# Performance work log

Measured on AMD Instinct MI355X. Metric: run time of the kernel, lower is better.

The kernel has to match this reference:

```python
import jax, jax.numpy as jnp
import numpy as np

D_MAIN = 256
D_INT = 512
N_FEAT = 128
N_CLASSES = 10
B = 1024
N_CAND = 100000
CTX = 96
EPS = 1e-5


def layer_norm(x, scale, bias):
    m = jnp.mean(x, axis=-1, keepdims=True)
    v = jnp.var(x, axis=-1, keepdims=True)
    return (x - m) / jnp.sqrt(v + EPS) * scale + bias


def setup_inputs() -> dict:
    key = jax.random.key(0)
    ks = jax.random.split(key, 16)

    def lin_w(k, fi, fo):
        return jax.random.uniform(k, (fi, fo), minval=-1.0, maxval=1.0, dtype=jnp.float32) / np.sqrt(fi)

    def lin_b(k, fi, fo):
        return jax.random.uniform(k, (fo,), minval=-1.0, maxval=1.0, dtype=jnp.float32) / np.sqrt(fi)

    return {
        "x_num": jax.random.normal(ks[0], (B, N_FEAT), dtype=jnp.float32),
        "cand_num": jax.random.normal(ks[1], (N_CAND, N_FEAT), dtype=jnp.float32),
        "cand_y": jax.random.randint(ks[2], (N_CAND,), 0, N_CLASSES),
        "context_size": CTX,
        # input linear (forward_E with encoder_n_blocks=0)
        "W_lin": lin_w(ks[3], N_FEAT, D_MAIN), "b_lin": lin_b(ks[3], N_FEAT, D_MAIN),
        # K projection
        "W_K": lin_w(ks[4], D_MAIN, D_MAIN), "b_K": lin_b(ks[4], D_MAIN, D_MAIN),
        # label embedding Y (init uniform(-1, 1) per reset_parameters)
        "Y_emb": jax.random.uniform(ks[5], (N_CLASSES, D_MAIN), minval=-1.0, maxval=1.0, dtype=jnp.float32),
        # T: Linear(d, d_int) -> ReLU -> Linear(d_int, d, bias=False)
        "T_W1": lin_w(ks[6], D_MAIN, D_INT), "T_b1": lin_b(ks[6], D_MAIN, D_INT),
        "T_W2": lin_w(ks[7], D_INT, D_MAIN),
        # predictor block (LayerNorm -> Linear -> ReLU -> Dropout -> Linear), residual
        "bp_ln_s": jnp.ones((D_MAIN,), jnp.float32), "bp_ln_b": jnp.zeros((D_MAIN,), jnp.float32),
        "bp_W1": lin_w(ks[8], D_MAIN, D_INT), "bp_b1": lin_b(ks[8], D_MAIN, D_INT),
        "bp_W2": lin_w(ks[9], D_INT, D_MAIN), "bp_b2": lin_b(ks[9], D_INT, D_MAIN),
        # head P: LayerNorm -> ReLU -> Linear(d, n_classes)
        "P_ln_s": jnp.ones((D_MAIN,), jnp.float32), "P_ln_b": jnp.zeros((D_MAIN,), jnp.float32),
        "P_W": lin_w(ks[10], D_MAIN, N_CLASSES), "P_b": lin_b(ks[10], D_MAIN, N_CLASSES),
    }


def reference(x_num, cand_num, cand_y, context_size,
              W_lin, b_lin, W_K, b_K, Y_emb, T_W1, T_b1, T_W2,
              bp_ln_s, bp_ln_b, bp_W1, bp_b1, bp_W2, bp_b2,
              P_ln_s, P_ln_b, P_W, P_b):
    # forward_E (encoder_n_blocks=0 => single Linear, normlization is None)
    x = x_num @ W_lin + b_lin                       # [B, d]
    k = x @ W_K + b_K                               # [B, d]

    # candidate keys computed under torch.no_grad in the original -> stop_gradient
    ki_all = jax.lax.stop_gradient((cand_num @ W_lin + b_lin) @ W_K + b_K)  # [N, d]

    # FAISS GpuIndexFlatL2 search: exact L2 top-k (smallest squared distance)
    d2 = (jnp.sum(k * k, axis=-1, keepdims=True)
          - 2.0 * (k @ ki_all.T)
          + jnp.sum(ki_all * ki_all, axis=-1))      # [B, N]
    _, I = jax.lax.top_k(-jax.lax.stop_gradient(d2), context_size)  # [B, C]

    ki = ki_all[I]                                  # [B, C, d]
    diff = k[:, None, :] - ki                       # [B, C, d]
    # NOTE: source computes S = -(-|k|^2 + 2 k.ki - |ki|^2) = +squared distance
    S = jnp.sum(diff * diff, axis=-1)               # [B, C]
    w = jax.nn.softmax(S, axis=-1)                  # context_dropout inactive at inference

    enc_y = Y_emb[cand_y[I]]                        # [B, C, d]
    V = enc_y + jax.nn.relu(diff @ T_W1 + T_b1) @ T_W2
    V = jnp.einsum('bc,bcd->bd', w, V)              # weighted aggregation

    x = x + V
    # predictor block (predictor_n_blocks=1)
    h = layer_norm(x, bp_ln_s, bp_ln_b)
    h = jax.nn.relu(h @ bp_W1 + bp_b1) @ bp_W2 + bp_b2
    x = x + h
    # head P
    return jax.nn.relu(layer_norm(x, P_ln_s, P_ln_b)) @ P_W + P_b
```

## Files before the change

kernel.cpp:

```cpp
#include <hip/hip_runtime.h>
#include <hip/hip_bf16.h>

#define B_ROWS   1024
#define N_FEAT   128
#define D_MAIN   256
#define D_INT    512
#define N_CAND   100000
#define CTX      96
#define N_CLS    10
#define PCHN     8192
#define N2       91808
#define RKEEP    128
#define SCAP     6144
#define SVSTRIDE 16

typedef __attribute__((ext_vector_type(8))) short bf16x8;
typedef __attribute__((ext_vector_type(4))) float f32x4;
typedef unsigned long long u64;

__device__ __forceinline__ float wsum(float v) {
    #pragma unroll
    for (int o = 32; o > 0; o >>= 1) v += __shfl_down(v, o);
    return v;
}
__device__ __forceinline__ float wmax(float v) {
    #pragma unroll
    for (int o = 32; o > 0; o >>= 1) v = fmaxf(v, __shfl_down(v, o));
    return v;
}
__device__ __forceinline__ float blockSum256(float v, float* red) {
    int t = threadIdx.x;
    float s = wsum(v);
    if ((t & 63) == 0) red[t >> 6] = s;
    __syncthreads();
    s = red[0] + red[1] + red[2] + red[3];
    __syncthreads();
    return s;
}
__device__ __forceinline__ float b2f(unsigned short u) {
    return __uint_as_float(((unsigned)u) << 16);
}
__device__ __forceinline__ unsigned short f2b(float f) {
    unsigned x = __float_as_uint(f);
    return (unsigned short)((x + 0x7fff + ((x >> 16) & 1)) >> 16);
}
__device__ __forceinline__ unsigned fkey(float f) {
    unsigned u = __float_as_uint(f);
    return u ^ ((((int)u >> 31)) | 0x80000000u);
}
__device__ __forceinline__ float finv(unsigned k) {
    unsigned u = (k & 0x80000000u) ? (k ^ 0x80000000u) : ~k;
    return __uint_as_float(u);
}
#define SPLIT1(x, hv, lv) { unsigned short _h = f2b(x); hv = (short)_h; lv = (short)f2b((x) - b2f(_h)); }

__global__ __launch_bounds__(256) void encode_batch(
    const float* __restrict__ xn, const float* __restrict__ Wl, const float* __restrict__ bl,
    const float* __restrict__ Wk, const float* __restrict__ bk,
    float* __restrict__ xout, float* __restrict__ kout, float* __restrict__ knorm)
{
    int b = blockIdx.x, t = threadIdx.x;
    __shared__ float si[128], sx[256], red[4];
    if (t < 128) si[t] = xn[b * N_FEAT + t];
    __syncthreads();
    float a = bl[t];
    for (int i = 0; i < 128; ++i) a += si[i] * Wl[i * D_MAIN + t];
    xout[b * D_MAIN + t] = a;
    sx[t] = a;
    __syncthreads();
    float a2 = bk[t];
    for (int i = 0; i < 256; ++i) a2 += sx[i] * Wk[i * D_MAIN + t];
    kout[b * D_MAIN + t] = a2;
    float s = blockSum256(a2 * a2, red);
    if (t == 0) knorm[b] = s;
}

__global__ __launch_bounds__(256) void fuse_weights(
    const float* __restrict__ Wl, const float* __restrict__ Wk,
    const float* __restrict__ bl, const float* __restrict__ bk,
    float* __restrict__ Wf, float* __restrict__ bf)
{
    int i = blockIdx.x, t = threadIdx.x;
    __shared__ float row[256];
    if (i < 128) {
        if (t < 128) row[t] = 0.f;
        row[t % 256] = 0.f;
        __syncthreads();
        if (t < 256) {  }
        row[t] = Wl[i * D_MAIN + t];
        __syncthreads();
        float a = 0.f;
        for (int k = 0; k < 256; ++k) a += row[k] * Wk[k * D_MAIN + t];
        Wf[i * D_MAIN + t] = a;
    } else {
        row[t] = bl[t];
        __syncthreads();
        float a = bk[t];
        for (int k = 0; k < 256; ++k) a += row[k] * Wk[k * D_MAIN + t];
        bf[t] = a;
    }
}

template<bool WRITE_BF16>
__global__ __launch_bounds__(256) void gemm_split3(
    const float* __restrict__ A,
    const unsigned short* __restrict__ Bh,
    const unsigned short* __restrict__ Bl,
    const float* __restrict__ bias,
    float* __restrict__ Cf,
    unsigned short* __restrict__ Cbf,
    int M, int N, int K)
{
    __shared__ __align__(16) short Ash[4096], Asl[4096];
    __shared__ __align__(16) short Bsh[2048], Bsl[2048];
    const int t = threadIdx.x;
    const int bm = blockIdx.x * 128, bn = blockIdx.y * 64;
    const int wave = t >> 6, lane = t & 63;
    const int wm = (wave >> 1) * 64, wn = (wave & 1) * 32;
    const int lr = lane & 15, lkg = lane >> 4;
    f32x4 acc[4][2] = {};
    const int row0 = t >> 2, kg0 = t & 3;
    const int row1 = row0 + 64;
    const int p0 = ((kg0 + (row0 >> 2)) & 3) ^ (row0 & 3);
    const int p1 = ((kg0 + (row1 >> 2)) & 3) ^ (row1 & 3);
    const int gm0 = bm + row0, gm1 = bm + row1;
    const int nB = bn + row0;

    float4 u00, u01, u10, u11;
    bf16x8 bh0, bl0;
    auto prefetch = [&](int kq) {
        float4 z4 = make_float4(0.f, 0.f, 0.f, 0.f); bf16x8 z = {};
        u00 = z4; u01 = z4; u10 = z4; u11 = z4;
        bh0 = z; bl0 = z;
        if (gm0 < M) {
            const float* ap = A + (size_t)gm0 * K + kq + kg0 * 8;
            u00 = *(const float4*)ap; u01 = *(const float4*)(ap + 4);
        }
        if (gm1 < M) {
            const float* ap = A + (size_t)gm1 * K + kq + kg0 * 8;
            u10 = *(const float4*)ap; u11 = *(const float4*)(ap + 4);
        }
        if (nB < N) {
            bh0 = *(const bf16x8*)(Bh + (size_t)nB * K + kq + kg0 * 8);
            bl0 = *(const bf16x8*)(Bl + (size_t)nB * K + kq + kg0 * 8);
        }
    };
    prefetch(0);

    for (int k0 = 0; k0 < K; k0 += 32) {
        bf16x8 a0h, a0l, a1h, a1l;
        SPLIT1(u00.x, a0h[0], a0l[0]); SPLIT1(u00.y, a0h[1], a0l[1]);
        SPLIT1(u00.z, a0h[2], a0l[2]); SPLIT1(u00.w, a0h[3], a0l[3]);
        SPLIT1(u01.x, a0h[4], a0l[4]); SPLIT1(u01.y, a0h[5], a0l[5]);
        SPLIT1(u01.z, a0h[6], a0l[6]); SPLIT1(u01.w, a0h[7], a0l[7]);
        SPLIT1(u10.x, a1h[0], a1l[0]); SPLIT1(u10.y, a1h[1], a1l[1]);
        SPLIT1(u10.z, a1h[2], a1l[2]); SPLIT1(u10.w, a1h[3], a1l[3]);
        SPLIT1(u11.x, a1h[4], a1l[4]); SPLIT1(u11.y, a1h[5], a1l[5]);
        SPLIT1(u11.z, a1h[6], a1l[6]); SPLIT1(u11.w, a1h[7], a1l[7]);
        __syncthreads();
        *(bf16x8*)&Ash[(row0 * 4 + p0) * 8] = a0h;
        *(bf16x8*)&Asl[(row0 * 4 + p0) * 8] = a0l;
        *(bf16x8*)&Ash[(row1 * 4 + p1) * 8] = a1h;
        *(bf16x8*)&Asl[(row1 * 4 + p1) * 8] = a1l;
        *(bf16x8*)&Bsh[(row0 * 4 + p0) * 8] = bh0;
        *(bf16x8*)&Bsl[(row0 * 4 + p0) * 8] = bl0;
        if (k0 + 32 < K) prefetch(k0 + 32);
        __syncthreads();
        bf16x8 bfh[2], bfl[2];
        #pragma unroll
        for (int n = 0; n < 2; ++n) {
            int r = wn + n * 16 + lr;
            int p = ((lkg + (r >> 2)) & 3) ^ (r & 3);
            bfh[n] = *(const bf16x8*)&Bsh[(r * 4 + p) * 8];
            bfl[n] = *(const bf16x8*)&Bsl[(r * 4 + p) * 8];
        }
        #pragma unroll
        for (int m = 0; m < 4; ++m) {
            int r = wm + m * 16 + lr;
            int p = ((lkg + (r >> 2)) & 3) ^ (r & 3);
            bf16x8 ah = *(const bf16x8*)&Ash[(r * 4 + p) * 8];
            bf16x8 al = *(const bf16x8*)&Asl[(r * 4 + p) * 8];
            #pragma unroll
            for (int n = 0; n < 2; ++n) {
                acc[m][n] = __builtin_amdgcn_mfma_f32_16x16x32_bf16(al, bfh[n], acc[m][n], 0, 0, 0);
                acc[m][n] = __builtin_amdgcn_mfma_f32_16x16x32_bf16(ah, bfl[n], acc[m][n], 0, 0, 0);
                acc[m][n] = __builtin_amdgcn_mfma_f32_16x16x32_bf16(ah, bfh[n], acc[m][n], 0, 0, 0);
            }
        }
    }
    #pragma unroll
    for (int m = 0; m < 4; ++m) {
        #pragma unroll
        for (int n = 0; n < 2; ++n) {
            f32x4 a = acc[m][n];
            int gcol = bn + wn + n * 16 + lr;
            if (gcol >= N) continue;
            float bv = bias[gcol];
            #pragma unroll
            for (int r = 0; r < 4; ++r) {
                int grow = bm + wm + m * 16 + lkg * 4 + r;
                if (grow >= M) continue;
                float v = a[r] + bv;
                Cf[(size_t)grow * N + gcol] = v;
                if (WRITE_BF16) Cbf[(size_t)grow * N + gcol] = f2b(v);
            }
        }
    }
}

template<bool RELU, bool OUT_BF16>
__global__ __launch_bounds__(256) void gemm_bf16(
    const unsigned short* __restrict__ A,
    const unsigned short* __restrict__ Bt,
    const float* __restrict__ bias,
    void* __restrict__ C, int M, int N, int K)
{
    __shared__ __align__(16) short As[4096];
    __shared__ __align__(16) short Bs[2048];
    const int t = threadIdx.x;
    const int bm = blockIdx.x * 128, bn = blockIdx.y * 64;
    const int wave = t >> 6, lane = t & 63;
    const int wm = (wave >> 1) * 64, wn = (wave & 1) * 32;
    const int lr = lane & 15, lkg = lane >> 4;
    f32x4 acc[4][2] = {};
    const int row0 = t >> 2, kg0 = t & 3;
    const int row1 = row0 + 64;
    const int p0 = ((kg0 + (row0 >> 2)) & 3) ^ (row0 & 3);
    const int p1 = ((kg0 + (row1 >> 2)) & 3) ^ (row1 & 3);
    const int gm0 = bm + row0, gm1 = bm + row1;
    const int nB = bn + row0;

    bf16x8 a0, a1, b0;
    auto prefetch = [&](int kq) {
        bf16x8 z = {};
        a0 = z; a1 = z; b0 = z;
        if (gm0 < M) a0 = *(const bf16x8*)(A + (size_t)gm0 * K + kq + kg0 * 8);
        if (gm1 < M) a1 = *(const bf16x8*)(A + (size_t)gm1 * K + kq + kg0 * 8);
        if (nB < N) b0 = *(const bf16x8*)(Bt + (size_t)nB * K + kq + kg0 * 8);
    };
    prefetch(0);

    for (int k0 = 0; k0 < K; k0 += 32) {
        __syncthreads();
        *(bf16x8*)&As[(row0 * 4 + p0) * 8] = a0;
        *(bf16x8*)&As[(row1 * 4 + p1) * 8] = a1;
        *(bf16x8*)&Bs[(row0 * 4 + p0) * 8] = b0;
        if (k0 + 32 < K) prefetch(k0 + 32);
        __syncthreads();
        bf16x8 bfr[2];
        #pragma unroll
        for (int n = 0; n < 2; ++n) {
            int r = wn + n * 16 + lr;
            int p = ((lkg + (r >> 2)) & 3) ^ (r & 3);
            bfr[n] = *(const bf16x8*)&Bs[(r * 4 + p) * 8];
        }
        #pragma unroll
        for (int m = 0; m < 4; ++m) {
            int r = wm + m * 16 + lr;
            int p = ((lkg + (r >> 2)) & 3) ^ (r & 3);
            bf16x8 af = *(const bf16x8*)&As[(r * 4 + p) * 8];
            #pragma unroll
            for (int n = 0; n < 2; ++n)
                acc[m][n] = __builtin_amdgcn_mfma_f32_16x16x32_bf16(
                    af, bfr[n], acc[m][n], 0, 0, 0);
        }
    }
    #pragma unroll
    for (int m = 0; m < 4; ++m) {
        #pragma unroll
        for (int n = 0; n < 2; ++n) {
            f32x4 a = acc[m][n];
            int gcol = bn + wn + n * 16 + lr;
            if (gcol >= N) continue;
            float bv = bias ? bias[gcol] : 0.f;
            #pragma unroll
            for (int r = 0; r < 4; ++r) {
                int grow = bm + wm + m * 16 + lkg * 4 + r;
                if (grow >= M) continue;
                float v = a[r] + bv;
                if (RELU) v = fmaxf(v, 0.f);
                if (OUT_BF16)
                    ((unsigned short*)C)[(size_t)grow * N + gcol] = f2b(v);
                else
                    ((float*)C)[(size_t)grow * N + gcol] = v;
            }
        }
    }
}

template<int MODE>
__global__ __launch_bounds__(256) void screen_gemm(
    const unsigned short* __restrict__ A,
    const unsigned short* __restrict__ Bt,
    float* __restrict__ scores,
    int N, int n0,
    const float* __restrict__ knrm,
    const unsigned* __restrict__ tau32, int* __restrict__ svcnt,
    u64* __restrict__ surv)
{
    __shared__ __align__(16) short As[4096];
    __shared__ __align__(16) short Bs[2048];
    const int t = threadIdx.x;
    const int bm = blockIdx.x * 128, bn = blockIdx.y * 64;
    const int wave = t >> 6, lane = t & 63;
    const int wm = (wave >> 1) * 64, wn = (wave & 1) * 32;
    const int lr = lane & 15, lkg = lane >> 4;
    f32x4 acc[4][2] = {};
    const int row0 = t >> 2, kg0 = t & 3;
    const int row1 = row0 + 64;
    const int p0 = ((kg0 + (row0 >> 2)) & 3) ^ (row0 & 3);
    const int p1 = ((kg0 + (row1 >> 2)) & 3) ^ (row1 & 3);
    const int gm0 = bm + row0, gm1 = bm + row1;
    const int nB = bn + row0;

    bf16x8 a0, a1, b0;
    auto prefetch = [&](int kq) {
        bf16x8 z = {};
        b0 = z;
        a0 = *(const bf16x8*)(A + (size_t)gm0 * D_MAIN + kq + kg0 * 8);
        a1 = *(const bf16x8*)(A + (size_t)gm1 * D_MAIN + kq + kg0 * 8);
        if (nB < N) b0 = *(const bf16x8*)(Bt + (size_t)nB * D_MAIN + kq + kg0 * 8);
    };
    prefetch(0);

    for (int k0 = 0; k0 < D_MAIN; k0 += 32) {
        __syncthreads();
        *(bf16x8*)&As[(row0 * 4 + p0) * 8] = a0;
        *(bf16x8*)&As[(row1 * 4 + p1) * 8] = a1;
        *(bf16x8*)&Bs[(row0 * 4 + p0) * 8] = b0;
        if (k0 + 32 < D_MAIN) prefetch(k0 + 32);
        __syncthreads();
        bf16x8 bfr[2];
        #pragma unroll
        for (int n = 0; n < 2; ++n) {
            int r = wn + n * 16 + lr;
            int p = ((lkg + (r >> 2)) & 3) ^ (r & 3);
            bfr[n] = *(const bf16x8*)&Bs[(r * 4 + p) * 8];
        }
        #pragma unroll
        for (int m = 0; m < 4; ++m) {
            int r = wm + m * 16 + lr;
            int p = ((lkg + (r >> 2)) & 3) ^ (r & 3);
            bf16x8 af = *(const bf16x8*)&As[(r * 4 + p) * 8];
            #pragma unroll
            for (int n = 0; n < 2; ++n)
                acc[m][n] = __builtin_amdgcn_mfma_f32_16x16x32_bf16(
                    af, bfr[n], acc[m][n], 0, 0, 0);
        }
    }

    float knv[2];
    #pragma unroll
    for (int n = 0; n < 2; ++n) {
        int gcol = bn + wn + n * 16 + lr;
        knv[n] = (gcol < N) ? knrm[gcol] : 0.f;
    }
    if (MODE == 1) {
        #pragma unroll
        for (int m = 0; m < 4; ++m) {
            #pragma unroll
            for (int n = 0; n < 2; ++n) {
                int gcol = bn + wn + n * 16 + lr;
                if (gcol >= N) continue;
                #pragma unroll
                for (int r = 0; r < 4; ++r) {
                    int grow = bm + wm + m * 16 + lkg * 4 + r;
                    scores[(size_t)grow * PCHN + gcol] = knv[n] - 2.0f * acc[m][n][r];
                }
            }
        }
    } else {
        unsigned taur[16];
        #pragma unroll
        for (int m = 0; m < 4; ++m)
            #pragma unroll
            for (int r = 0; r < 4; ++r)
                taur[m * 4 + r] = tau32[bm + wm + m * 16 + lkg * 4 + r];
        #pragma unroll
        for (int m = 0; m < 4; ++m) {
            #pragma unroll
            for (int r = 0; r < 4; ++r) {
                int grow = bm + wm + m * 16 + lkg * 4 + r;
                #pragma unroll
                for (int n = 0; n < 2; ++n) {
                    int gcol = bn + wn + n * 16 + lr;
                    bool pass = false;
                    unsigned key = 0;
                    if (gcol < N) {
                        key = fkey(knv[n] - 2.0f * acc[m][n][r]);
                        pass = key <= taur[m * 4 + r];
                    }
                    u64 bal = __ballot(pass);
                    unsigned g16 = (unsigned)((bal >> (lkg * 16)) & 0xFFFFu);
                    if (g16) {
                        int cntp = __popc(g16);
                        int first = __ffs(g16) - 1;
                        int base = 0;
                        if (lr == first) base = atomicAdd(&svcnt[grow * SVSTRIDE], cntp);
                        base = __shfl(base, lkg * 16 + first);
                        if (pass) {
                            int p = base + __popc(g16 & ((1u << lr) - 1u));
                            if (p < SCAP)
                                surv[(size_t)grow * SCAP + p] =
                                    ((u64)key << 32) | (unsigned)(n0 + gcol);
                        }
                    }
                }
            }
        }
    }
}

__global__ __launch_bounds__(256) void cvt_f32_bf16_vec(
    const float* __restrict__ in, unsigned short* __restrict__ out, int n4)
{
    int i = blockIdx.x * 256 + threadIdx.x;
    if (i >= n4) return;
    float4 v = ((const float4*)in)[i];
    ushort4 u;
    u.x = f2b(v.x); u.y = f2b(v.y); u.z = f2b(v.z); u.w = f2b(v.w);
    ((ushort4*)out)[i] = u;
}
__global__ __launch_bounds__(256) void cvt_transpose(
    const float* __restrict__ W, unsigned short* __restrict__ Wt, int K, int N)
{
    int idx = blockIdx.x * 256 + threadIdx.x;
    if (idx >= K * N) return;
    int k = idx / N, n = idx % N;
    Wt[(size_t)n * K + k] = f2b(W[idx]);
}
__global__ __launch_bounds__(256) void cvt_split_transpose(
    const float* __restrict__ W, unsigned short* __restrict__ Wh,
    unsigned short* __restrict__ Wl, int K, int N)
{
    int idx = blockIdx.x * 256 + threadIdx.x;
    if (idx >= K * N) return;
    int k = idx / N, n = idx % N;
    float v = W[idx];
    unsigned short h = f2b(v);
    Wh[(size_t)n * K + k] = h;
    Wl[(size_t)n * K + k] = f2b(v - b2f(h));
}

__global__ __launch_bounds__(256) void rownorms(const float* __restrict__ ki,
                                                float* __restrict__ out, int M)
{
    int n = blockIdx.x * 4 + (threadIdx.x >> 6);
    int lane = threadIdx.x & 63;
    if (n >= M) return;
    float4 v = *(const float4*)(ki + (size_t)n * D_MAIN + lane * 4);
    float s = v.x * v.x + v.y * v.y + v.z * v.z + v.w * v.w;
    s = wsum(s);
    if (lane == 0) out[n] = s;
}

__device__ void bitonic512(u64* s, int t)
{
    for (int k = 2; k <= 512; k <<= 1) {
        for (int j = k >> 1; j > 0; j >>= 1) {
            __syncthreads();
            #pragma unroll
            for (int q = 0; q < 2; ++q) {
                int l = t + q * 256;
                int p = l ^ j;
                if (p > l) {
                    u64 a = s[l], bb = s[p];
                    bool up = ((l & k) == 0);
                    if ((a > bb) == up) { s[l] = bb; s[p] = a; }
                }
            }
        }
    }
    __syncthreads();
}
__device__ void bitonic1024(u64* s, int t)
{
    for (int k = 2; k <= 1024; k <<= 1) {
        for (int j = k >> 1; j > 0; j >>= 1) {
            __syncthreads();
            #pragma unroll
            for (int q = 0; q < 4; ++q) {
                int l = t + q * 256;
                int p = l ^ j;
                if (p > l) {
                    u64 a = s[l], bb = s[p];
                    bool up = ((l & k) == 0);
                    if ((a > bb) == up) { s[l] = bb; s[p] = a; }
                }
            }
        }
    }
    __syncthreads();
}

__global__ __launch_bounds__(256) void pilot_select(
    const float* __restrict__ scores, u64* __restrict__ pilotbuf,
    unsigned* __restrict__ tau32)
{
    int b = blockIdx.x, t = threadIdx.x;
    int lane = t & 63;
    __shared__ u64 s[1024];
    __shared__ int cnt;
    __shared__ u64 tauf;
    const float* row = scores + (size_t)b * PCHN;
    #pragma unroll
    for (int q = 0; q < 4; ++q) {
        int n = t + q * 256;
        s[n] = ((u64)fkey(row[n]) << 32) | (unsigned)n;
    }
    __syncthreads();
    bitonic1024(s, t);
    if (t == 0) { cnt = 128; tauf = s[127]; }
    #pragma unroll
    for (int q = 0; q < 4; ++q) { int n = t + q * 256; if (n >= 128) s[n] = ~0ULL; }
    __syncthreads();
    for (int base = 1024; base < PCHN; base += 1024) {
        u64 tau = tauf;
        int n = base + t * 4;
        float4 v = *(const float4*)(row + n);
        #pragma unroll
        for (int j = 0; j < 4; ++j) {
            float x = (&v.x)[j];
            u64 e = ((u64)fkey(x) << 32) | (unsigned)(n + j);
            bool pass = e < tau;
            u64 m = __ballot(pass);
            if (m) {
                int bs = 0;
                if (lane == 0) bs = atomicAdd(&cnt, (int)__popcll(m));
                bs = __shfl(bs, 0);
                if (pass) {
                    int p = bs + (int)__popcll(m & ((1ULL << lane) - 1ULL));
                    if (p < 1024) s[p] = e;
                }
            }
        }
        __syncthreads();
        if (cnt > 512) {
            bitonic1024(s, t);
            if (t == 0) { cnt = 128; tauf = s[127]; }
            #pragma unroll
            for (int q = 0; q < 4; ++q) { int n2 = t + q * 256; if (n2 >= 128) s[n2] = ~0ULL; }
        }
        __syncthreads();
    }
    bitonic1024(s, t);
    if (t < 128) pilotbuf[(size_t)b * 128 + t] = s[t];
    if (t == 0) tau32[b] = (unsigned)(s[127] >> 32);
}

__global__ __launch_bounds__(128) void init_surv(
    const u64* __restrict__ pilotbuf, u64* __restrict__ surv, int* __restrict__ svcnt)
{
    int b = blockIdx.x, t = threadIdx.x;
    surv[(size_t)b * SCAP + t] = pilotbuf[(size_t)b * 128 + t];
    if (t == 0) svcnt[b * SVSTRIDE] = 128;
}

__global__ __launch_bounds__(256) void final_select(
    const u64* __restrict__ surv, const int* __restrict__ svcnt,
    int* __restrict__ refI)
{
    int b = blockIdx.x, t = threadIdx.x;
    int lane = t & 63;
    __shared__ u64 s[1024];
    __shared__ int cnt;
    __shared__ u64 tauf;
    int total = svcnt[b * SVSTRIDE]; if (total > SCAP) total = SCAP;
    const u64* rowp = surv + (size_t)b * SCAP;
    #pragma unroll
    for (int q = 0; q < 4; ++q) {
        int n = t + q * 256;
        s[n] = (n < total) ? rowp[n] : ~0ULL;
    }
    __syncthreads();
    bitonic1024(s, t);
    if (t == 0) { cnt = 128; tauf = s[127]; }
    #pragma unroll
    for (int q = 0; q < 4; ++q) { int n = t + q * 256; if (n >= 128) s[n] = ~0ULL; }
    __syncthreads();
    for (int base = 1024; base < total; base += 1024) {
        u64 tau = tauf;
        int n = base + t * 4;
        #pragma unroll
        for (int j = 0; j < 4; ++j) {
            u64 e = (n + j < total) ? rowp[n + j] : ~0ULL;
            bool pass = e < tau;
            u64 m = __ballot(pass);
            if (m) {
                int bs = 0;
                if (lane == 0) bs = atomicAdd(&cnt, (int)__popcll(m));
                bs = __shfl(bs, 0);
                if (pass) {
                    int p = bs + (int)__popcll(m & ((1ULL << lane) - 1ULL));
                    if (p < 1024) s[p] = e;
                }
            }
        }
        __syncthreads();
        if (cnt > 512) {
            bitonic1024(s, t);
            if (t == 0) { cnt = 128; tauf = s[127]; }
            #pragma unroll
            for (int q = 0; q < 4; ++q) { int n2 = t + q * 256; if (n2 >= 128) s[n2] = ~0ULL; }
        }
        __syncthreads();
    }
    bitonic1024(s, t);
    if (t < RKEEP) refI[b * RKEEP + t] = (int)(unsigned)(s[t] & 0xffffffffULL);
}

__global__ __launch_bounds__(256) void refine(
    const float* __restrict__ kmat, const float* __restrict__ kiall,
    const float* __restrict__ knorm, const float* __restrict__ kinorm,
    const int* __restrict__ refI, int* __restrict__ Ifin, float* __restrict__ Sbuf)
{
    int b = blockIdx.x, t = threadIdx.x;
    int w = t >> 6, lane = t & 63;
    __shared__ float kk[256];
    __shared__ u64 s[512];
    kk[t] = kmat[b * D_MAIN + t];
    s[t] = ~0ULL; s[t + 256] = ~0ULL;
    __syncthreads();
    float kn = knorm[b];
    for (int sv = w; sv < RKEEP; sv += 4) {
        int n = refI[b * RKEEP + sv];
        float4 a = *(const float4*)&kk[lane * 4];
        float4 bb = ((const float4*)(kiall + (size_t)n * D_MAIN))[lane];
        float d = a.x * bb.x + a.y * bb.y + a.z * bb.z + a.w * bb.w;
        d = wsum(d);
        if (lane == 0) {
            float d2 = kn + kinorm[n] - 2.f * d;
            s[sv] = ((u64)fkey(d2) << 32) | (unsigned)n;
        }
    }
    __syncthreads();
    bitonic512(s, t);
    if (t < CTX) {
        u64 e = s[t];
        Ifin[b * CTX + t] = (int)(unsigned)(e & 0xffffffffULL);
        Sbuf[b * CTX + t] = finv((unsigned)(e >> 32));
    }
}

__global__ __launch_bounds__(64) void gather_diff_bf(
    const float* __restrict__ kmat, const float* __restrict__ kiall,
    const int* __restrict__ I, unsigned short* __restrict__ diffb)
{
    int bc = blockIdx.x;
    int b = bc / CTX;
    int t = threadIdx.x;
    int idx = I[bc];
    float4 kv = ((const float4*)(kmat + (size_t)b * D_MAIN))[t];
    float4 iv = ((const float4*)(kiall + (size_t)idx * D_MAIN))[t];
    ushort4 u;
    u.x = f2b(kv.x - iv.x); u.y = f2b(kv.y - iv.y);
    u.z = f2b(kv.z - iv.z); u.w = f2b(kv.w - iv.w);
    ((ushort4*)(diffb + (size_t)bc * D_MAIN))[t] = u;
}

__global__ __launch_bounds__(128) void softmax96(const float* __restrict__ S,
                                                 float* __restrict__ w)
{
    int b = blockIdx.x, t = threadIdx.x;
    __shared__ float rm[2], rs[2];
    float v = (t < CTX) ? S[b * CTX + t] : -__builtin_inff();
    float m = wmax(v);
    if ((t & 63) == 0) rm[t >> 6] = m;
    __syncthreads();
    m = fmaxf(rm[0], rm[1]);
    float e = (t < CTX) ? expf(v - m) : 0.f;
    float ss = wsum(e);
    if ((t & 63) == 0) rs[t >> 6] = ss;
    __syncthreads();
    float Z = rs[0] + rs[1];
    if (t < CTX) w[b * CTX + t] = e / Z;
}

__global__ __launch_bounds__(256) void aggregate(
    const float* __restrict__ w, const int* __restrict__ I,
    const int* __restrict__ cand_y, const float* __restrict__ Yemb,
    const float* __restrict__ mlp, const float* __restrict__ x,
    float* __restrict__ x2)
{
    int b = blockIdx.x, t = threadIdx.x;
    __shared__ float ws[CTX];
    __shared__ int lab[CTX];
    if (t < CTX) {
        ws[t] = w[b * CTX + t];
        lab[t] = cand_y[I[b * CTX + t]];
    }
    __syncthreads();
    float acc = 0.f;
    for (int c = 0; c < CTX; ++c) {
        acc += ws[c] * (Yemb[lab[c] * D_MAIN + t] + mlp[((size_t)b * CTX + c) * D_MAIN + t]);
    }
    x2[b * D_MAIN + t] = x[b * D_MAIN + t] + acc;
}

__global__ __launch_bounds__(256) void predictor_head(
    const float* __restrict__ x2,
    const float* __restrict__ lns, const float* __restrict__ lnb,
    const float* __restrict__ W1, const float* __restrict__ b1,
    const float* __restrict__ W2, const float* __restrict__ b2,
    const float* __restrict__ plns, const float* __restrict__ plnb,
    const float* __restrict__ PW, const float* __restrict__ Pb,
    float* __restrict__ out)
{
    int b = blockIdx.x, t = threadIdx.x;
    __shared__ float ln1[256], hdn[512], red[4];
    float xv = x2[b * D_MAIN + t];
    float s1 = blockSum256(xv, red);
    float s2 = blockSum256(xv * xv, red);
    float mean = s1 * (1.f / 256.f);
    float var = s2 * (1.f / 256.f) - mean * mean;
    float rstd = rsqrtf(var + 1e-5f);
    ln1[t] = (xv - mean) * rstd * lns[t] + lnb[t];
    __syncthreads();
    #pragma unroll
    for (int rep = 0; rep < 2; ++rep) {
        int j = t + rep * 256;
        float a = b1[j];
        for (int i = 0; i < 256; ++i) a += ln1[i] * W1[i * D_INT + j];
        hdn[j] = fmaxf(a, 0.f);
    }
    __syncthreads();
    float a3 = b2[t];
    for (int i = 0; i < 512; ++i) a3 += hdn[i] * W2[i * D_MAIN + t];
    float x3 = xv + a3;
    float s3 = blockSum256(x3, red);
    float s4 = blockSum256(x3 * x3, red);
    float m2 = s3 * (1.f / 256.f);
    float v2 = s4 * (1.f / 256.f) - m2 * m2;
    float r2 = rsqrtf(v2 + 1e-5f);
    float rv = fmaxf((x3 - m2) * r2 * plns[t] + plnb[t], 0.f);
    __syncthreads();
    ln1[t] = rv;
    __syncthreads();
    if (t < N_CLS) {
        float a = Pb[t];
        for (int i = 0; i < 256; ++i) a += ln1[i] * PW[i * N_CLS + t];
        out[b * N_CLS + t] = a;
    }
}

extern "C" void kernel_launch(void* const* d_in, const int* in_sizes, int n_in,
                              void* d_out, int out_size, void* d_ws, size_t ws_size,
                              hipStream_t stream)
{
    (void)in_sizes; (void)n_in; (void)out_size; (void)ws_size;
    const float* x_num   = (const float*)d_in[0];
    const float* cand    = (const float*)d_in[1];
    const int*   cand_y  = (const int*)d_in[2];
    const float* W_lin   = (const float*)d_in[4];
    const float* b_lin   = (const float*)d_in[5];
    const float* W_K     = (const float*)d_in[6];
    const float* b_K     = (const float*)d_in[7];
    const float* Y_emb   = (const float*)d_in[8];
    const float* T_W1    = (const float*)d_in[9];
    const float* T_b1    = (const float*)d_in[10];
    const float* T_W2    = (const float*)d_in[11];
    const float* bp_ln_s = (const float*)d_in[12];
    const float* bp_ln_b = (const float*)d_in[13];
    const float* bp_W1   = (const float*)d_in[14];
    const float* bp_b1   = (const float*)d_in[15];
    const float* bp_W2   = (const float*)d_in[16];
    const float* bp_b2   = (const float*)d_in[17];
    const float* P_ln_s  = (const float*)d_in[18];
    const float* P_ln_b  = (const float*)d_in[19];
    const float* P_W     = (const float*)d_in[20];
    const float* P_b     = (const float*)d_in[21];
    float* outp = (float*)d_out;

    char* ws = (char*)d_ws;
    float* kiall  = (float*)(ws + 0);
    unsigned short* hidden = (unsigned short*)(ws + 0);
    unsigned short* ki_bf = (unsigned short*)(ws + 102400000);
    unsigned short* diffb = (unsigned short*)(ws + 102400000);
    float* mlpbuf = (float*)(ws + 102400000);
    float* scores = (float*)(ws + 153600000);
    u64*   surv   = (u64*)(ws + 153600000);
    const size_t T = 204800000;
    float* xbuf   = (float*)(ws + T + 0);
    float* kbuf   = (float*)(ws + T + 1048576);
    float* x2buf  = (float*)(ws + T + 2097152);
    float* knorm  = (float*)(ws + T + 3145728);
    float* kinorm = (float*)(ws + T + 3149824);
    unsigned short* k_bf = (unsigned short*)(ws + T + 3551232);
    float* Wf     = (float*)(ws + T + 4075520);
    unsigned short* WfH = (unsigned short*)(ws + T + 4206592);
    unsigned short* WfL = (unsigned short*)(ws + T + 4272128);
    float* bfused = (float*)(ws + T + 4337664);
    unsigned short* W1t  = (unsigned short*)(ws + T + 4468736);
    unsigned short* W2t  = (unsigned short*)(ws + T + 4730880);
    float* Sbuf   = (float*)(ws + T + 4993024);
    float* wbuf   = (float*)(ws + T + 5386240);
    int*   refI   = (int*)(ws + T + 5779456);
    int*   Ifin   = (int*)(ws + T + 6303744);
    u64*   pilotbuf = (u64*)(ws + T + 6696960);
    unsigned* tau32 = (unsigned*)(ws + T + 7745536);
    int*   svcnt  = (int*)(ws + T + 7749632);

    encode_batch<<<B_ROWS, 256, 0, stream>>>(x_num, W_lin, b_lin, W_K, b_K,
                                             xbuf, kbuf, knorm);
    fuse_weights<<<129, 256, 0, stream>>>(W_lin, W_K, b_lin, b_K, Wf, bfused);
    cvt_split_transpose<<<128, 256, 0, stream>>>(Wf, WfH, WfL, N_FEAT, D_MAIN);
    cvt_transpose<<<512, 256, 0, stream>>>(T_W1, W1t, D_MAIN, D_INT);
    cvt_transpose<<<512, 256, 0, stream>>>(T_W2, W2t, D_INT, D_MAIN);
    cvt_f32_bf16_vec<<<256, 256, 0, stream>>>(kbuf, k_bf, B_ROWS * D_MAIN / 4);
    gemm_split3<true><<<dim3(782, 4), 256, 0, stream>>>(
        cand, WfH, WfL, bfused, kiall, ki_bf, N_CAND, D_MAIN, N_FEAT);
    rownorms<<<25000, 256, 0, stream>>>(kiall, kinorm, N_CAND);
    screen_gemm<1><<<dim3(8, PCHN / 64), 256, 0, stream>>>(
        k_bf, ki_bf, scores, PCHN, 0, kinorm, nullptr, nullptr, nullptr);
    pilot_select<<<B_ROWS, 256, 0, stream>>>(scores, pilotbuf, tau32);
    init_surv<<<B_ROWS, 128, 0, stream>>>(pilotbuf, surv, svcnt);
    screen_gemm<2><<<dim3(8, (N2 + 63) / 64), 256, 0, stream>>>(
        k_bf, ki_bf + (size_t)PCHN * D_MAIN, nullptr, N2, PCHN,
        kinorm + PCHN, tau32, svcnt, surv);
    final_select<<<B_ROWS, 256, 0, stream>>>(surv, svcnt, refI);
    refine<<<B_ROWS, 256, 0, stream>>>(kbuf, kiall, knorm, kinorm, refI, Ifin, Sbuf);
    softmax96<<<B_ROWS, 128, 0, stream>>>(Sbuf, wbuf);
    gather_diff_bf<<<B_ROWS * CTX, 64, 0, stream>>>(kbuf, kiall, Ifin, diffb);
    gemm_bf16<true, true><<<dim3(768, 8), 256, 0, stream>>>(
        diffb, W1t, T_b1, hidden, B_ROWS * CTX, D_INT, D_MAIN);
    gemm_bf16<false, false><<<dim3(768, 4), 256, 0, stream>>>(
        hidden, W2t, nullptr, mlpbuf, B_ROWS * CTX, D_MAIN, D_INT);
    aggregate<<<B_ROWS, 256, 0, stream>>>(wbuf, Ifin, cand_y, Y_emb, mlpbuf,
                                          xbuf, x2buf);
    predictor_head<<<B_ROWS, 256, 0, stream>>>(x2buf, bp_ln_s, bp_ln_b,
                                               bp_W1, bp_b1, bp_W2, bp_b2,
                                               P_ln_s, P_ln_b, P_W, P_b, outp);
}
```

Before: 811.0 us.

## Double-buffer LDS tiles in bf16 GEMM and screening kernels

Switches the shared-memory A/B tiles in gemm_bf16 and screen_gemm to two buffers. Each iteration now stores the next tile while MFMAs consume the current one, which halves the per-iteration barriers from two to one. It also removes redundant zeroing and a barrier in fuse_weights. The cost is doubled LDS use per block, which may reduce occupancy.

```diff
diff --git a/kernel.cpp b/kernel.cpp
--- a/kernel.cpp
+++ b/kernel.cpp
@@ -83,10 +83,6 @@
     int i = blockIdx.x, t = threadIdx.x;
     __shared__ float row[256];
     if (i < 128) {
-        if (t < 128) row[t] = 0.f;
-        row[t % 256] = 0.f;
-        __syncthreads();
-        if (t < 256) {  }
         row[t] = Wl[i * D_MAIN + t];
         __syncthreads();
         float a = 0.f;
@@ -215,8 +211,8 @@
     const float* __restrict__ bias,
     void* __restrict__ C, int M, int N, int K)
 {
-    __shared__ __align__(16) short As[4096];
-    __shared__ __align__(16) short Bs[2048];
+    __shared__ __align__(16) short As[2][4096];
+    __shared__ __align__(16) short Bs[2][2048];
     const int t = threadIdx.x;
     const int bm = blockIdx.x * 128, bn = blockIdx.y * 64;
     const int wave = t >> 6, lane = t & 63;
@@ -239,31 +235,39 @@
         if (nB < N) b0 = *(const bf16x8*)(Bt + (size_t)nB * K + kq + kg0 * 8);
     };
     prefetch(0);
+    *(bf16x8*)&As[0][(row0 * 4 + p0) * 8] = a0;
+    *(bf16x8*)&As[0][(row1 * 4 + p1) * 8] = a1;
+    *(bf16x8*)&Bs[0][(row0 * 4 + p0) * 8] = b0;
+    if (32 < K) prefetch(32);
+    __syncthreads();
 
     for (int k0 = 0; k0 < K; k0 += 32) {
-        __syncthreads();
-        *(bf16x8*)&As[(row0 * 4 + p0) * 8] = a0;
-        *(bf16x8*)&As[(row1 * 4 + p1) * 8] = a1;
-        *(bf16x8*)&Bs[(row0 * 4 + p0) * 8] = b0;
-        if (k0 + 32 < K) prefetch(k0 + 32);
-        __syncthreads();
+        const int cur = (k0 >> 5) & 1;
+        if (k0 + 32 < K) {
+            const int nxt = cur ^ 1;
+            *(bf16x8*)&As[nxt][(row0 * 4 + p0) * 8] = a0;
+            *(bf16x8*)&As[nxt][(row1 * 4 + p1) * 8] = a1;
+            *(bf16x8*)&Bs[nxt][(row0 * 4 + p0) * 8] = b0;
+            if (k0 + 64 < K) prefetch(k0 + 64);
+        }
         bf16x8 bfr[2];
         #pragma unroll
         for (int n = 0; n < 2; ++n) {
             int r = wn + n * 16 + lr;
             int p = ((lkg + (r >> 2)) & 3) ^ (r & 3);
-            bfr[n] = *(const bf16x8*)&Bs[(r * 4 + p) * 8];
+            bfr[n] = *(const bf16x8*)&Bs[cur][(r * 4 + p) * 8];
         }
         #pragma unroll
         for (int m = 0; m < 4; ++m) {
             int r = wm + m * 16 + lr;
             int p = ((lkg + (r >> 2)) & 3) ^ (r & 3);
-            bf16x8 af = *(const bf16x8*)&As[(r * 4 + p) * 8];
+            bf16x8 af = *(const bf16x8*)&As[cur][(r * 4 + p) * 8];
             #pragma unroll
             for (int n = 0; n < 2; ++n)
                 acc[m][n] = __builtin_amdgcn_mfma_f32_16x16x32_bf16(
                     af, bfr[n], acc[m][n], 0, 0, 0);
         }
+        __syncthreads();
     }
     #pragma unroll
     for (int m = 0; m < 4; ++m) {
@@ -298,8 +302,8 @@
     const unsigned* __restrict__ tau32, int* __restrict__ svcnt,
     u64* __restrict__ surv)
 {
-    __shared__ __align__(16) short As[4096];
-    __shared__ __align__(16) short Bs[2048];
+    __shared__ __align__(16) short As[2][4096];
+    __shared__ __align__(16) short Bs[2][2048];
     const int t = threadIdx.x;
     const int bm = blockIdx.x * 128, bn = blockIdx.y * 64;
     const int wave = t >> 6, lane = t & 63;
@@ -322,31 +326,39 @@
         if (nB < N) b0 = *(const bf16x8*)(Bt + (size_t)nB * D_MAIN + kq + kg0 * 8);
     };
     prefetch(0);
+    *(bf16x8*)&As[0][(row0 * 4 + p0) * 8] = a0;
+    *(bf16x8*)&As[0][(row1 * 4 + p1) * 8] = a1;
+    *(bf16x8*)&Bs[0][(row0 * 4 + p0) * 8] = b0;
+    prefetch(32);
+    __syncthreads();
 
     for (int k0 = 0; k0 < D_MAIN; k0 += 32) {
-        __syncthreads();
-        *(bf16x8*)&As[(row0 * 4 + p0) * 8] = a0;
-        *(bf16x8*)&As[(row1 * 4 + p1) * 8] = a1;
-        *(bf16x8*)&Bs[(row0 * 4 + p0) * 8] = b0;
-        if (k0 + 32 < D_MAIN) prefetch(k0 + 32);
-        __syncthreads();
+        const int cur = (k0 >> 5) & 1;
+        if (k0 + 32 < D_MAIN) {
+            const int nxt = cur ^ 1;
+            *(bf16x8*)&As[nxt][(row0 * 4 + p0) * 8] = a0;
+            *(bf16x8*)&As[nxt][(row1 * 4 + p1) * 8] = a1;
+            *(bf16x8*)&Bs[nxt][(row0 * 4 + p0) * 8] = b0;
+            if (k0 + 64 < D_MAIN) prefetch(k0 + 64);
+        }
         bf16x8 bfr[2];
         #pragma unroll
         for (int n = 0; n < 2; ++n) {
             int r = wn + n * 16 + lr;
             int p = ((lkg + (r >> 2)) & 3) ^ (r & 3);
-            bfr[n] = *(const bf16x8*)&Bs[(r * 4 + p) * 8];
+            bfr[n] = *(const bf16x8*)&Bs[cur][(r * 4 + p) * 8];
         }
         #pragma unroll
         for (int m = 0; m < 4; ++m) {
             int r = wm + m * 16 + lr;
             int p = ((lkg + (r >> 2)) & 3) ^ (r & 3);
-            bf16x8 af = *(const bf16x8*)&As[(r * 4 + p) * 8];
+            bf16x8 af = *(const bf16x8*)&As[cur][(r * 4 + p) * 8];
             #pragma unroll
             for (int n = 0; n < 2; ++n)
                 acc[m][n] = __builtin_amdgcn_mfma_f32_16x16x32_bf16(
                     af, bfr[n], acc[m][n], 0, 0, 0);
         }
+        __syncthreads();
     }
 
     float knv[2];
```

After: 802.1 us. Within noise of the previous version (-1.1%).
